# Kernel tuning notes

Measured on AMD Instinct MI355X. Metric: run time of the kernel, lower is better.

## Reference

```python
import jax, jax.numpy as jnp
import numpy as np

H, DH, HID = 8, 16, 128
N_USER, N_ITEM, N_TASTE, N_IMAGE = 20000, 50000, 50000, 50000


def setup_inputs() -> dict:
    key = jax.random.key(0)
    ks = jax.random.split(key, 24)
    f = jax.random.normal
    s = 1.0 / np.sqrt(HID).astype(np.float32)
    inp = {
        "x_user": f(ks[0], (N_USER, HID), jnp.float32),
        "x_item": f(ks[1], (N_ITEM, HID), jnp.float32),
        "x_taste": f(ks[2], (N_TASTE, HID), jnp.float32),
        "x_image": f(ks[3], (N_IMAGE, HID), jnp.float32),
        "Wk": f(ks[4], (4, HID, HID), jnp.float32) * s,
        "bk": jnp.zeros((4, HID), jnp.float32),
        "Wq": f(ks[5], (4, HID, HID), jnp.float32) * s,
        "bq": jnp.zeros((4, HID), jnp.float32),
        "Wv": f(ks[6], (4, HID, HID), jnp.float32) * s,
        "bv": jnp.zeros((4, HID), jnp.float32),
        "a_rel": f(ks[7], (4, H, DH, DH), jnp.float32) * (1.0 / np.sqrt(DH).astype(np.float32)),
        "m_rel": f(ks[8], (4, H, DH, DH), jnp.float32) * (1.0 / np.sqrt(DH).astype(np.float32)),
        "p_rel": jnp.ones((4, H), jnp.float32),
        "Wo": f(ks[9], (2, HID, HID), jnp.float32) * s,
        "bo": jnp.zeros((2, HID), jnp.float32),
        "skip": jnp.ones((2,), jnp.float32),
        "ti_src": jax.random.randint(ks[10], (50000,), 0, N_TASTE, jnp.int32),
        "ti_dst": jax.random.randint(ks[11], (50000,), 0, N_ITEM, jnp.int32),
        "im_src": jax.random.randint(ks[12], (50000,), 0, N_IMAGE, jnp.int32),
        "im_dst": jax.random.randint(ks[13], (50000,), 0, N_ITEM, jnp.int32),
        "ub_src": jax.random.randint(ks[14], (500000,), 0, N_USER, jnp.int32),
        "ub_dst": jax.random.randint(ks[15], (500000,), 0, N_ITEM, jnp.int32),
        "bu_src": jax.random.randint(ks[16], (500000,), 0, N_ITEM, jnp.int32),
        "bu_dst": jax.random.randint(ks[17], (500000,), 0, N_USER, jnp.int32),
    }
    return inp


def _kqv(x, i, Wk, bk, Wq, bq, Wv, bv):
    k = (x @ Wk[i] + bk[i]).reshape(-1, H, DH)
    q = (x @ Wq[i] + bq[i]).reshape(-1, H, DH)
    v = (x @ Wv[i] + bv[i]).reshape(-1, H, DH)
    return k, q, v


def _edge_alpha_msg(k_src, v_src, q_dst, src, dst, a, m, p):
    # per-edge-type relation transform at node level, then gather per edge
    kr = jnp.einsum('nhd,hde->nhe', k_src, a)  # [Nsrc,H,DH]
    vr = jnp.einsum('nhd,hde->nhe', v_src, m)
    alpha = (q_dst[dst] * kr[src]).sum(-1) * p * (1.0 / np.sqrt(DH).astype(np.float32))  # [E,H]
    return alpha, vr[src]


def _seg_softmax_agg(alpha, msg, dst, n):
    amax = jax.ops.segment_max(alpha, dst, num_segments=n)
    amax = jnp.where(jnp.isfinite(amax), amax, 0.0)
    ex = jnp.exp(alpha - amax[dst])
    den = jax.ops.segment_sum(ex, dst, num_segments=n)
    w = ex / (den[dst] + 1e-16)
    return jax.ops.segment_sum(msg * w[..., None], dst, num_segments=n)  # [n,H,DH]


def reference(x_user, x_item, x_taste, x_image, Wk, bk, Wq, bq, Wv, bv,
              a_rel, m_rel, p_rel, Wo, bo, skip,
              ti_src, ti_dst, im_src, im_dst, ub_src, ub_dst, bu_src, bu_dst):
    k_u, q_u, v_u = _kqv(x_user, 0, Wk, bk, Wq, bq, Wv, bv)
    k_i, q_i, v_i = _kqv(x_item, 1, Wk, bk, Wq, bq, Wv, bv)
    k_t, _, v_t = _kqv(x_taste, 2, Wk, bk, Wq, bq, Wv, bv)
    k_g, _, v_g = _kqv(x_image, 3, Wk, bk, Wq, bq, Wv, bv)

    # edges into 'item': taste(0), image(1), user-buys(2); softmax over all combined per item
    a0, m0 = _edge_alpha_msg(k_t, v_t, q_i, ti_src, ti_dst, a_rel[0], m_rel[0], p_rel[0])
    a1, m1 = _edge_alpha_msg(k_g, v_g, q_i, im_src, im_dst, a_rel[1], m_rel[1], p_rel[1])
    a2, m2 = _edge_alpha_msg(k_u, v_u, q_i, ub_src, ub_dst, a_rel[2], m_rel[2], p_rel[2])
    alpha_i = jnp.concatenate([a0, a1, a2], 0)
    msg_i = jnp.concatenate([m0, m1, m2], 0)
    dst_i = jnp.concatenate([ti_dst, im_dst, ub_dst], 0)
    agg_i = _seg_softmax_agg(alpha_i, msg_i, dst_i, N_ITEM)

    # edges into 'user': item-bought_by(3)
    a3, m3 = _edge_alpha_msg(k_i, v_i, q_u, bu_src, bu_dst, a_rel[3], m_rel[3], p_rel[3])
    agg_u = _seg_softmax_agg(a3, m3, bu_dst, N_USER)

    out_i = jax.nn.gelu(agg_i.reshape(-1, HID), approximate=False) @ Wo[0] + bo[0]
    g_i = jax.nn.sigmoid(skip[0])
    out_i = g_i * out_i + (1.0 - g_i) * x_item

    out_u = jax.nn.gelu(agg_u.reshape(-1, HID), approximate=False) @ Wo[1] + bo[1]
    g_u = jax.nn.sigmoid(skip[1])
    out_u = g_u * out_u + (1.0 - g_u) * x_user
    return (out_i, out_u)
```

## Files before the change

kernel.cpp:

```cpp
#include <hip/hip_runtime.h>
#include <math.h>


namespace {
constexpr int HIDN  = 128;
constexpr int NHEAD = 8;

constexpr int NU = 20000, NI = 50000, NT = 50000, NG = 50000;
constexpr int E_TI = 50000, E_IM = 50000, E_UB = 500000, E_BU = 500000;
constexpr int ETOT = E_TI + E_IM + E_UB + E_BU;
constexpr int ND   = NI + NU;

constexpr int BASE_U = 0;
constexpr int BASE_I = NU;
constexpr int BASE_T = NU + NI;
constexpr int BASE_G = NU + NI + NT;

constexpr int NMAT = 12;
constexpr int MATSZ = 128 * 128;
constexpr int SU = 136;

constexpr int NBU = (NU + 63) / 64;
constexpr int NBI = (NI + 63) / 64;
constexpr int NBT = (NT + 63) / 64;
constexpr int NBG = (NG + 63) / 64;
}

typedef __attribute__((ext_vector_type(8))) short short8v;
typedef __attribute__((ext_vector_type(4))) float f32x4;
typedef __attribute__((ext_vector_type(4))) unsigned short ushort4v;

__device__ __forceinline__ unsigned short bf16rne(float f) {
    unsigned u = __float_as_uint(f);
    unsigned r = (u + 0x7fffu + ((u >> 16) & 1u)) >> 16;
    return (unsigned short)r;
}
__device__ __forceinline__ float bf16f(unsigned short h) {
    return __uint_as_float(((unsigned)h) << 16);
}
__device__ __forceinline__ float bflo(unsigned int u) { return __uint_as_float(u << 16); }
__device__ __forceinline__ float bfhi(unsigned int u) { return __uint_as_float(u & 0xffff0000u); }

__global__ void build_cw_kernel(const float* __restrict__ Wk, const float* __restrict__ bk,
                                const float* __restrict__ Wv, const float* __restrict__ bv,
                                const float* __restrict__ a_rel, const float* __restrict__ m_rel,
                                const float* __restrict__ p_rel,
                                float* __restrict__ cw)
{
    const int total = 2 * 4 * 129 * 128;
    int idx = blockIdx.x * blockDim.x + threadIdx.x;
    if (idx >= total) return;
    int c     = idx & 127;
    int r     = (idx >> 7) % 129;
    int t     = ((idx >> 7) / 129) & 3;
    int which = idx / (4 * 129 * 128);
    const int et_map[4] = {2, 3, 0, 1};
    int et = et_map[t];
    const float* W = (which == 0 ? Wk : Wv) + (size_t)t * HIDN * HIDN;
    const float* b = (which == 0 ? bk : bv) + (size_t)t * HIDN;
    const float* A = (which == 0 ? a_rel : m_rel) + (size_t)et * NHEAD * 16 * 16;
    int h = c >> 4, e2 = c & 15;
    float s = 0.f;
#pragma unroll
    for (int d = 0; d < 16; ++d) {
        float w = (r == 128) ? b[h * 16 + d] : W[(size_t)r * HIDN + h * 16 + d];
        s = fmaf(w, A[h * 256 + d * 16 + e2], s);
    }
    if (which == 0) s *= p_rel[et * NHEAD + h] * 0.25f;
    cw[idx] = s;
}

__global__ void pack_kernel(const float* __restrict__ cw,
                            const float* __restrict__ Wq, const float* __restrict__ bq,
                            const float* __restrict__ Wo, const float* __restrict__ bo,
                            short* __restrict__ pkh, short* __restrict__ pkl,
                            float* __restrict__ bias)
{
    const int total = NMAT * MATSZ + NMAT * HIDN;
    int idx = blockIdx.x * blockDim.x + threadIdx.x;
    if (idx >= total) return;
    if (idx < NMAT * MATSZ) {
        int mat = idx >> 14;
        int rem = idx & (MATSZ - 1);
        int i    = rem & 7;
        int lane = (rem >> 3) & 63;
        int ct   = (rem >> 9) & 7;
        int ks   = rem >> 12;
        int k   = ks * 32 + ((lane >> 4) & 3) * 8 + i;
        int col = ct * 16 + (lane & 15);
        float v;
        if (mat < 8)       v = cw[(size_t)mat * 129 * 128 + (size_t)k * 128 + col];
        else if (mat < 10) v = Wq[(size_t)(mat - 8) * MATSZ + (size_t)k * 128 + col];
        else               v = Wo[(size_t)(mat - 10) * MATSZ + (size_t)k * 128 + col];
        unsigned short hb = bf16rne(v);
        float rest = v - bf16f(hb);
        pkh[idx] = (short)hb;
        pkl[idx] = (short)bf16rne(rest);
    } else {
        int b = idx - NMAT * MATSZ;
        int mat = b >> 7, col = b & 127;
        float v;
        if (mat < 8)       v = cw[(size_t)mat * 129 * 128 + (size_t)128 * 128 + col];
        else if (mat < 10) v = bq[(mat - 8) * HIDN + col];
        else               v = bo[(mat - 10) * HIDN + col];
        bias[b] = v;
    }
}

__global__ __launch_bounds__(256) void mfma_proj_all(
    const float* __restrict__ xu, const float* __restrict__ xi,
    const float* __restrict__ xt, const float* __restrict__ xg,
    const short* __restrict__ pkh, const short* __restrict__ pkl,
    const float* __restrict__ bias,
    unsigned short* __restrict__ krb, unsigned short* __restrict__ vrb,
    unsigned short* __restrict__ qb_u, unsigned short* __restrict__ qb_i)
{
    int b = blockIdx.x;
    int seg, bloc;
    if (b < NBU)                  { seg = 0; bloc = b; }
    else if (b < NBU + NBI)       { seg = 1; bloc = b - NBU; }
    else if (b < NBU + NBI + NBT) { seg = 2; bloc = b - NBU - NBI; }
    else                          { seg = 3; bloc = b - NBU - NBI - NBT; }
    const float* x = (seg == 0) ? xu : (seg == 1) ? xi : (seg == 2) ? xt : xg;
    const int M     = (seg == 0) ? NU : (seg == 1) ? NI : (seg == 2) ? NT : NG;
    const int rbase = (seg == 0) ? BASE_U : (seg == 1) ? BASE_I : (seg == 2) ? BASE_T : BASE_G;
    unsigned short* qp = (seg == 0) ? qb_u : (seg == 1) ? qb_i : nullptr;

    __shared__ unsigned short hs[64 * SU];
    __shared__ unsigned short ls[64 * SU];
    const int t  = threadIdx.x;
    const int r0 = bloc * 64;
    const int rows = min(64, M - r0);

#pragma unroll
    for (int p = 0; p < 8; ++p) {
        int f = p * 256 + t;
        int row = f >> 5, c4 = f & 31;
        float4 v = make_float4(0.f, 0.f, 0.f, 0.f);
        if (row < rows) v = *(const float4*)(x + (size_t)(r0 + row) * HIDN + c4 * 4);
        float vv[4] = {v.x, v.y, v.z, v.w};
        ushort4v hq, lq;
#pragma unroll
        for (int i = 0; i < 4; ++i) {
            unsigned short hb = bf16rne(vv[i]);
            hq[i] = hb;
            lq[i] = bf16rne(vv[i] - bf16f(hb));
        }
        *(ushort4v*)&hs[row * SU + c4 * 4] = hq;
        *(ushort4v*)&ls[row * SU + c4 * 4] = lq;
    }
    __syncthreads();

    const int l = t & 63, w = t >> 6;
    const int kgrp = l >> 4;
    const int ct0  = 2 * w;
    const int ccol = l & 15;

    for (int mi = 0; mi < 3; ++mi) {
        if (mi == 2 && qp == nullptr) break;
        const int mat = (mi == 0) ? seg : (mi == 1) ? (4 + seg) : (8 + seg);
        const short8v* bh = (const short8v*)(pkh + (size_t)mat * MATSZ);
        const short8v* bl = (const short8v*)(pkl + (size_t)mat * MATSZ);
        const float*   bs = bias + mat * HIDN;

        short8v B1[4][2], B2[4][2];
#pragma unroll
        for (int ks = 0; ks < 4; ++ks) {
#pragma unroll
            for (int c = 0; c < 2; ++c) {
                B1[ks][c] = bh[(ks * 8 + ct0 + c) * 64 + l];
                if (mi == 2) B2[ks][c] = bl[(ks * 8 + ct0 + c) * 64 + l];
            }
        }

        const float bv0 = bs[(ct0 + 0) * 16 + ccol];
        const float bv1 = bs[(ct0 + 1) * 16 + ccol];

        for (int rt = 0; rt < 4; ++rt) {
            f32x4 a0, a1;
            a0[0]=0.f;a0[1]=0.f;a0[2]=0.f;a0[3]=0.f;
            a1[0]=0.f;a1[1]=0.f;a1[2]=0.f;a1[3]=0.f;
            const int arow = rt * 16 + ccol;
#pragma unroll
            for (int ks = 0; ks < 4; ++ks) {
                short8v ah = *(const short8v*)&hs[arow * SU + ks * 32 + kgrp * 8];
                short8v al = *(const short8v*)&ls[arow * SU + ks * 32 + kgrp * 8];
                a0 = __builtin_amdgcn_mfma_f32_16x16x32_bf16(ah, B1[ks][0], a0, 0, 0, 0);
                a1 = __builtin_amdgcn_mfma_f32_16x16x32_bf16(ah, B1[ks][1], a1, 0, 0, 0);
                a0 = __builtin_amdgcn_mfma_f32_16x16x32_bf16(al, B1[ks][0], a0, 0, 0, 0);
                a1 = __builtin_amdgcn_mfma_f32_16x16x32_bf16(al, B1[ks][1], a1, 0, 0, 0);
                if (mi == 2) {
                    a0 = __builtin_amdgcn_mfma_f32_16x16x32_bf16(ah, B2[ks][0], a0, 0, 0, 0);
                    a1 = __builtin_amdgcn_mfma_f32_16x16x32_bf16(ah, B2[ks][1], a1, 0, 0, 0);
                }
            }
            const int crow = r0 + rt * 16 + kgrp * 4;
            unsigned short* dst = (mi == 0) ? krb + (size_t)rbase * HIDN
                                : (mi == 1) ? vrb + (size_t)rbase * HIDN
                                            : qp;
#pragma unroll
            for (int j = 0; j < 4; ++j) {
                int grow = crow + j;
                if (grow < M) {
                    size_t o = (size_t)grow * HIDN;
                    dst[o + (ct0 + 0) * 16 + ccol] = bf16rne(a0[j] + bv0);
                    dst[o + (ct0 + 1) * 16 + ccol] = bf16rne(a1[j] + bv1);
                }
            }
        }
    }
}

__global__ __launch_bounds__(256) void mfma_out_all(
    const float* __restrict__ agg_i, const float* __restrict__ agg_u,
    const short* __restrict__ pkh, const short* __restrict__ pkl,
    const float* __restrict__ bias,
    const float* __restrict__ x_item, const float* __restrict__ x_user,
    const float* __restrict__ skip_ptr,
    float* __restrict__ outp)
{
    int b = blockIdx.x;
    int seg = (b < NBI) ? 0 : 1;
    int bloc = (seg == 0) ? b : b - NBI;
    const float* agg = (seg == 0) ? agg_i : agg_u;
    const float* xin = (seg == 0) ? x_item : x_user;
    const int M = (seg == 0) ? NI : NU;
    const int mat = 10 + seg;
    float* out = (seg == 0) ? outp : outp + (size_t)NI * HIDN;

    __shared__ unsigned short hs[64 * SU];
    __shared__ unsigned short ls[64 * SU];
    const int t  = threadIdx.x;
    const int r0 = bloc * 64;
    const int rows = min(64, M - r0);

#pragma unroll
    for (int p = 0; p < 8; ++p) {
        int f = p * 256 + t;
        int row = f >> 5, c4 = f & 31;
        float4 v = make_float4(0.f, 0.f, 0.f, 0.f);
        if (row < rows) v = *(const float4*)(agg + (size_t)(r0 + row) * HIDN + c4 * 4);
        float vv[4] = {v.x, v.y, v.z, v.w};
        ushort4v hq, lq;
#pragma unroll
        for (int i = 0; i < 4; ++i) {
            float g = 0.5f * vv[i] * (1.0f + erff(vv[i] * 0.70710678118654752440f));
            unsigned short hb = bf16rne(g);
            hq[i] = hb;
            lq[i] = bf16rne(g - bf16f(hb));
        }
        *(ushort4v*)&hs[row * SU + c4 * 4] = hq;
        *(ushort4v*)&ls[row * SU + c4 * 4] = lq;
    }
    __syncthreads();

    const int l = t & 63, w = t >> 6;
    const int kgrp = l >> 4;
    const int ct0  = 2 * w;
    const int ccol = l & 15;

    const short8v* bh = (const short8v*)(pkh + (size_t)mat * MATSZ);
    const short8v* bl = (const short8v*)(pkl + (size_t)mat * MATSZ);
    const float*   bs = bias + mat * HIDN;

    short8v B1[4][2], B2[4][2];
#pragma unroll
    for (int ks = 0; ks < 4; ++ks) {
#pragma unroll
        for (int c = 0; c < 2; ++c) {
            B1[ks][c] = bh[(ks * 8 + ct0 + c) * 64 + l];
            B2[ks][c] = bl[(ks * 8 + ct0 + c) * 64 + l];
        }
    }

    const float gate = 1.f / (1.f + expf(-skip_ptr[seg]));
    const float og = 1.f - gate;
    const float bv0 = bs[(ct0 + 0) * 16 + ccol];
    const float bv1 = bs[(ct0 + 1) * 16 + ccol];

    for (int rt = 0; rt < 4; ++rt) {
        f32x4 a0, a1;
        a0[0]=0.f;a0[1]=0.f;a0[2]=0.f;a0[3]=0.f;
        a1[0]=0.f;a1[1]=0.f;a1[2]=0.f;a1[3]=0.f;
        const int arow = rt * 16 + ccol;
#pragma unroll
        for (int ks = 0; ks < 4; ++ks) {
            short8v ah = *(const short8v*)&hs[arow * SU + ks * 32 + kgrp * 8];
            short8v al = *(const short8v*)&ls[arow * SU + ks * 32 + kgrp * 8];
            a0 = __builtin_amdgcn_mfma_f32_16x16x32_bf16(ah, B1[ks][0], a0, 0, 0, 0);
            a1 = __builtin_amdgcn_mfma_f32_16x16x32_bf16(ah, B1[ks][1], a1, 0, 0, 0);
            a0 = __builtin_amdgcn_mfma_f32_16x16x32_bf16(al, B1[ks][0], a0, 0, 0, 0);
            a1 = __builtin_amdgcn_mfma_f32_16x16x32_bf16(al, B1[ks][1], a1, 0, 0, 0);
            a0 = __builtin_amdgcn_mfma_f32_16x16x32_bf16(ah, B2[ks][0], a0, 0, 0, 0);
            a1 = __builtin_amdgcn_mfma_f32_16x16x32_bf16(ah, B2[ks][1], a1, 0, 0, 0);
        }
        const int crow = r0 + rt * 16 + kgrp * 4;
#pragma unroll
        for (int j = 0; j < 4; ++j) {
            int grow = crow + j;
            if (grow < M) {
                size_t o = (size_t)grow * HIDN;
                size_t o0 = o + (ct0 + 0) * 16 + ccol;
                size_t o1 = o + (ct0 + 1) * 16 + ccol;
                out[o0] = gate * (a0[j] + bv0) + og * xin[o0];
                out[o1] = gate * (a1[j] + bv1) + og * xin[o1];
            }
        }
    }
}


__global__ void hist_kernel(const int* __restrict__ ti_dst, const int* __restrict__ im_dst,
                            const int* __restrict__ ub_dst, const int* __restrict__ bu_dst,
                            int* __restrict__ deg)
{
    int i = blockIdx.x * blockDim.x + threadIdx.x;
    if (i >= ETOT) return;
    int d;
    if (i < E_TI)                     d = ti_dst[i];
    else if (i < E_TI + E_IM)         d = im_dst[i - E_TI];
    else if (i < E_TI + E_IM + E_UB)  d = ub_dst[i - E_TI - E_IM];
    else                              d = NI + bu_dst[i - E_TI - E_IM - E_UB];
    atomicAdd(&deg[d], 1);
}

__global__ void scan1_kernel(int* __restrict__ deg, int* __restrict__ tops, int n)
{
    __shared__ int sh[256];
    int i = blockIdx.x * 256 + threadIdx.x;
    int v = (i < n) ? deg[i] : 0;
    sh[threadIdx.x] = v;
    __syncthreads();
    for (int o = 1; o < 256; o <<= 1) {
        int t = (threadIdx.x >= o) ? sh[threadIdx.x - o] : 0;
        __syncthreads();
        sh[threadIdx.x] += t;
        __syncthreads();
    }
    if (i < n) deg[i] = sh[threadIdx.x];
    if (threadIdx.x == 255) tops[blockIdx.x] = sh[255];
}

__global__ void scan2_kernel(int* __restrict__ tops, int nb)
{
    __shared__ int sh[1024];
    int v = (threadIdx.x < nb) ? tops[threadIdx.x] : 0;
    sh[threadIdx.x] = v;
    __syncthreads();
    for (int o = 1; o < 1024; o <<= 1) {
        int t = (threadIdx.x >= o) ? sh[threadIdx.x - o] : 0;
        __syncthreads();
        sh[threadIdx.x] += t;
        __syncthreads();
    }
    if (threadIdx.x < nb) tops[threadIdx.x] = sh[threadIdx.x];
}

__global__ void scan3_kernel(const int* __restrict__ part, const int* __restrict__ tops,
                             int* __restrict__ rowptr, int* __restrict__ cursor, int n)
{
    int i = blockIdx.x * 256 + threadIdx.x;
    if (i >= n) return;
    int add = (blockIdx.x > 0) ? tops[blockIdx.x - 1] : 0;
    int prev = (i > 0) ? ((threadIdx.x > 0) ? part[i - 1] + add
                                            : ((blockIdx.x > 0) ? tops[blockIdx.x - 1] : 0))
                       : 0;
    rowptr[i + 1] = part[i] + add;
    cursor[i] = prev;
    if (i == 0) rowptr[0] = 0;
}

__global__ void scatter_kernel(const int* __restrict__ ti_src, const int* __restrict__ ti_dst,
                               const int* __restrict__ im_src, const int* __restrict__ im_dst,
                               const int* __restrict__ ub_src, const int* __restrict__ ub_dst,
                               const int* __restrict__ bu_src, const int* __restrict__ bu_dst,
                               int* __restrict__ cursor, int* __restrict__ col)
{
    int i = blockIdx.x * blockDim.x + threadIdx.x;
    if (i >= ETOT) return;
    int d, row;
    if (i < E_TI)                    { d = ti_dst[i];                  row = BASE_T + ti_src[i]; }
    else if (i < E_TI + E_IM)        { int e = i - E_TI;               row = BASE_G + im_src[e]; d = im_dst[e]; }
    else if (i < E_TI + E_IM + E_UB) { int e = i - E_TI - E_IM;        row = BASE_U + ub_src[e]; d = ub_dst[e]; }
    else                             { int e = i - E_TI - E_IM - E_UB; row = BASE_I + bu_src[e]; d = NI + bu_dst[e]; }
    int p = atomicAdd(&cursor[d], 1);
    col[p] = row;
}

__global__ __launch_bounds__(256) void f12_kernel(
    const int* __restrict__ rowptr, const int* __restrict__ rowend,
    const int* __restrict__ col,
    const unsigned int* __restrict__ krw,
    const unsigned int* __restrict__ qb_i, const unsigned int* __restrict__ qb_u,
    const unsigned int* __restrict__ vrw,
    float* __restrict__ agg_i, float* __restrict__ agg_u)
{
    int wid = (blockIdx.x << 2) + (threadIdx.x >> 6);
    if (wid >= ND) return;
    const int l = threadIdx.x & 63;

    unsigned int qu = (wid < NI) ? qb_i[(size_t)wid * 64 + l]
                                 : qb_u[(size_t)(wid - NI) * 64 + l];
    const float qx = bflo(qu), qy = bfhi(qu);

    const int start = rowptr[wid], end = rowend[wid];
    float m = -3.0e38f, ax = 0.f, ay = 0.f, den = 0.f;

    int p = start;
    for (; p + 3 < end; p += 4) {
        int r0_ = col[p], r1_ = col[p + 1], r2_ = col[p + 2], r3_ = col[p + 3];
        unsigned int u0 = krw[(size_t)r0_ * 64 + l];
        unsigned int u1 = krw[(size_t)r1_ * 64 + l];
        unsigned int u2 = krw[(size_t)r2_ * 64 + l];
        unsigned int u3 = krw[(size_t)r3_ * 64 + l];
        unsigned int v0 = vrw[(size_t)r0_ * 64 + l];
        unsigned int v1 = vrw[(size_t)r1_ * 64 + l];
        unsigned int v2 = vrw[(size_t)r2_ * 64 + l];
        unsigned int v3 = vrw[(size_t)r3_ * 64 + l];
        float d0 = qx * bflo(u0) + qy * bfhi(u0);
        float d1 = qx * bflo(u1) + qy * bfhi(u1);
        float d2 = qx * bflo(u2) + qy * bfhi(u2);
        float d3 = qx * bflo(u3) + qy * bfhi(u3);
        d0 += __shfl_xor(d0, 1); d1 += __shfl_xor(d1, 1);
        d2 += __shfl_xor(d2, 1); d3 += __shfl_xor(d3, 1);
        d0 += __shfl_xor(d0, 2); d1 += __shfl_xor(d1, 2);
        d2 += __shfl_xor(d2, 2); d3 += __shfl_xor(d3, 2);
        d0 += __shfl_xor(d0, 4); d1 += __shfl_xor(d1, 4);
        d2 += __shfl_xor(d2, 4); d3 += __shfl_xor(d3, 4);
        float mn = fmaxf(m, fmaxf(fmaxf(d0, d1), fmaxf(d2, d3)));
        float s  = __expf(m - mn);
        float e0 = __expf(d0 - mn);
        float e1 = __expf(d1 - mn);
        float e2 = __expf(d2 - mn);
        float e3 = __expf(d3 - mn);
        ax = ax * s + e0 * bflo(v0) + e1 * bflo(v1) + e2 * bflo(v2) + e3 * bflo(v3);
        ay = ay * s + e0 * bfhi(v0) + e1 * bfhi(v1) + e2 * bfhi(v2) + e3 * bfhi(v3);
        den = den * s + (e0 + e1) + (e2 + e3);
        m = mn;
    }
    for (; p < end; ++p) {
        int r0_ = col[p];
        unsigned int u0 = krw[(size_t)r0_ * 64 + l];
        unsigned int v0 = vrw[(size_t)r0_ * 64 + l];
        float d0 = qx * bflo(u0) + qy * bfhi(u0);
        d0 += __shfl_xor(d0, 1);
        d0 += __shfl_xor(d0, 2);
        d0 += __shfl_xor(d0, 4);
        float mn = fmaxf(m, d0);
        float s  = __expf(m - mn);
        float e0 = __expf(d0 - mn);
        ax = ax * s + e0 * bflo(v0);
        ay = ay * s + e0 * bfhi(v0);
        den = den * s + e0;
        m = mn;
    }

    float inv = 1.f / (den + 1e-16f);
    float* dst = (wid < NI) ? agg_i + (size_t)wid * HIDN
                            : agg_u + (size_t)(wid - NI) * HIDN;
    *(float2*)(dst + 2 * l) = make_float2(ax * inv, ay * inv);
}

extern "C" void kernel_launch(void* const* d_in, const int* in_sizes, int n_in,
                              void* d_out, int out_size, void* d_ws, size_t ws_size,
                              hipStream_t stream)
{
    const float* x_user = (const float*)d_in[0];
    const float* x_item = (const float*)d_in[1];
    const float* x_taste= (const float*)d_in[2];
    const float* x_image= (const float*)d_in[3];
    const float* Wk     = (const float*)d_in[4];
    const float* bk     = (const float*)d_in[5];
    const float* Wq     = (const float*)d_in[6];
    const float* bq     = (const float*)d_in[7];
    const float* Wv     = (const float*)d_in[8];
    const float* bv     = (const float*)d_in[9];
    const float* a_rel  = (const float*)d_in[10];
    const float* m_rel  = (const float*)d_in[11];
    const float* p_rel  = (const float*)d_in[12];
    const float* Wo     = (const float*)d_in[13];
    const float* bo     = (const float*)d_in[14];
    const float* skip   = (const float*)d_in[15];
    const int* ti_src = (const int*)d_in[16];
    const int* ti_dst = (const int*)d_in[17];
    const int* im_src = (const int*)d_in[18];
    const int* im_dst = (const int*)d_in[19];
    const int* ub_src = (const int*)d_in[20];
    const int* ub_dst = (const int*)d_in[21];
    const int* bu_src = (const int*)d_in[22];
    const int* bu_dst = (const int*)d_in[23];

    float* ws = (float*)d_ws;
    float* outp = (float*)d_out;
    (void)in_sizes; (void)n_in; (void)out_size;

    size_t off = 0;
    auto alloc = [&](size_t n) { size_t o = off; off += n; return o; };
    const size_t o_cw   = alloc((size_t)2 * 4 * 129 * 128);
    const size_t o_pkh  = alloc((size_t)NMAT * MATSZ / 2);
    const size_t o_pkl  = alloc((size_t)NMAT * MATSZ / 2);
    const size_t o_bias = alloc((size_t)NMAT * HIDN);
    const size_t o_krb  = alloc((size_t)(NU + NI + NT + NG) * HIDN / 2);
    const size_t o_vrb  = alloc((size_t)(NU + NI + NT + NG) * HIDN / 2);
    const size_t o_q_i  = alloc((size_t)NI * HIDN / 2);
    const size_t o_q_u  = alloc((size_t)NU * HIDN / 2);
    const size_t o_agg  = alloc((size_t)(NI + NU) * HIDN);
    const size_t o_int  = alloc((size_t)(ND + 1) + ND + 1024 + ETOT);

    if (ws_size < off * sizeof(float)) return;

    unsigned short* krb  = (unsigned short*)(ws + o_krb);
    unsigned short* vrb  = (unsigned short*)(ws + o_vrb);
    unsigned short* qb_i = (unsigned short*)(ws + o_q_i);
    unsigned short* qb_u = (unsigned short*)(ws + o_q_u);

    short* pkh  = (short*)(ws + o_pkh);
    short* pkl  = (short*)(ws + o_pkl);
    float* bias = ws + o_bias;

    int* deg    = (int*)(ws + o_cw);
    int* rowptr = (int*)(ws + o_int);
    int* cursor = rowptr + (ND + 1);
    int* tops   = cursor + ND;
    int* col    = tops + 1024;

    float* agg_i = ws + o_agg;
    float* agg_u = ws + o_agg + (size_t)NI * HIDN;

    {
        int total = 2 * 4 * 129 * 128;
        build_cw_kernel<<<(total + 255) / 256, 256, 0, stream>>>(
            Wk, bk, Wv, bv, a_rel, m_rel, p_rel, ws + o_cw);
        int ptotal = NMAT * MATSZ + NMAT * HIDN;
        pack_kernel<<<(ptotal + 255) / 256, 256, 0, stream>>>(
            ws + o_cw, Wq, bq, Wo, bo, pkh, pkl, bias);
    }

    mfma_proj_all<<<NBU + NBI + NBT + NBG, 256, 0, stream>>>(
        x_user, x_item, x_taste, x_image, pkh, pkl, bias,
        krb, vrb, qb_u, qb_i);

    hipMemsetAsync(deg, 0, ND * sizeof(int), stream);
    hist_kernel<<<(ETOT + 255) / 256, 256, 0, stream>>>(ti_dst, im_dst, ub_dst, bu_dst, deg);
    const int NB1 = (ND + 255) / 256;
    scan1_kernel<<<NB1, 256, 0, stream>>>(deg, tops, ND);
    scan2_kernel<<<1, 1024, 0, stream>>>(tops, NB1);
    scan3_kernel<<<NB1, 256, 0, stream>>>(deg, tops, rowptr, cursor, ND);
    scatter_kernel<<<(ETOT + 255) / 256, 256, 0, stream>>>(
        ti_src, ti_dst, im_src, im_dst, ub_src, ub_dst, bu_src, bu_dst, cursor, col);

    const int NBW = (ND + 3) / 4;
    f12_kernel<<<NBW, 256, 0, stream>>>(
        rowptr, cursor, col,
        (const unsigned int*)krb, (const unsigned int*)qb_i, (const unsigned int*)qb_u,
        (const unsigned int*)vrb,
        agg_i, agg_u);

    mfma_out_all<<<NBI + NBU, 256, 0, stream>>>(
        agg_i, agg_u, pkh, pkl, bias, x_item, x_user, skip, outp);
}
```

Measured before the change: 328.4 us.

## Fuse weight-build, memset and histogram into other kernels; store aggregates as bf16

The relation-weight composition now happens inside the pack kernel, and the degree memset is folded into that same kernel, which drops a launch and a memset. The edge-degree histogram runs as extra blocks appended to the projection kernel, so it overlaps with the GEMM work. The aggregation output is stored in bf16 instead of fp32, halving its write and read traffic. The bf16 rounding of the aggregates adds precision loss before the output projection.

```diff
diff --git a/kernel.cpp b/kernel.cpp
--- a/kernel.cpp
+++ b/kernel.cpp
@@ -24,6 +24,8 @@
 constexpr int NBI = (NI + 63) / 64;
 constexpr int NBT = (NT + 63) / 64;
 constexpr int NBG = (NG + 63) / 64;
+constexpr int NPROJ = NBU + NBI + NBT + NBG;
+constexpr int NBH   = (ETOT + 255) / 256;
 }
 
 typedef __attribute__((ext_vector_type(8))) short short8v;
@@ -41,45 +43,19 @@
 __device__ __forceinline__ float bflo(unsigned int u) { return __uint_as_float(u << 16); }
 __device__ __forceinline__ float bfhi(unsigned int u) { return __uint_as_float(u & 0xffff0000u); }
 
-__global__ void build_cw_kernel(const float* __restrict__ Wk, const float* __restrict__ bk,
-                                const float* __restrict__ Wv, const float* __restrict__ bv,
-                                const float* __restrict__ a_rel, const float* __restrict__ m_rel,
-                                const float* __restrict__ p_rel,
-                                float* __restrict__ cw)
-{
-    const int total = 2 * 4 * 129 * 128;
-    int idx = blockIdx.x * blockDim.x + threadIdx.x;
-    if (idx >= total) return;
-    int c     = idx & 127;
-    int r     = (idx >> 7) % 129;
-    int t     = ((idx >> 7) / 129) & 3;
-    int which = idx / (4 * 129 * 128);
-    const int et_map[4] = {2, 3, 0, 1};
-    int et = et_map[t];
-    const float* W = (which == 0 ? Wk : Wv) + (size_t)t * HIDN * HIDN;
-    const float* b = (which == 0 ? bk : bv) + (size_t)t * HIDN;
-    const float* A = (which == 0 ? a_rel : m_rel) + (size_t)et * NHEAD * 16 * 16;
-    int h = c >> 4, e2 = c & 15;
-    float s = 0.f;
-#pragma unroll
-    for (int d = 0; d < 16; ++d) {
-        float w = (r == 128) ? b[h * 16 + d] : W[(size_t)r * HIDN + h * 16 + d];
-        s = fmaf(w, A[h * 256 + d * 16 + e2], s);
-    }
-    if (which == 0) s *= p_rel[et * NHEAD + h] * 0.25f;
-    cw[idx] = s;
-}
-
-__global__ void pack_kernel(const float* __restrict__ cw,
+__global__ void pack_kernel(const float* __restrict__ Wk, const float* __restrict__ bk,
+                            const float* __restrict__ Wv, const float* __restrict__ bv,
+                            const float* __restrict__ a_rel, const float* __restrict__ m_rel,
+                            const float* __restrict__ p_rel,
                             const float* __restrict__ Wq, const float* __restrict__ bq,
                             const float* __restrict__ Wo, const float* __restrict__ bo,
                             short* __restrict__ pkh, short* __restrict__ pkl,
-                            float* __restrict__ bias)
-{
-    const int total = NMAT * MATSZ + NMAT * HIDN;
+                            float* __restrict__ bias, int* __restrict__ deg)
+{
+    const int NW = NMAT * MATSZ;
+    const int NB = NMAT * HIDN;
     int idx = blockIdx.x * blockDim.x + threadIdx.x;
-    if (idx >= total) return;
-    if (idx < NMAT * MATSZ) {
+    if (idx < NW) {
         int mat = idx >> 14;
         int rem = idx & (MATSZ - 1);
         int i    = rem & 7;
@@ -89,21 +65,51 @@
         int k   = ks * 32 + ((lane >> 4) & 3) * 8 + i;
         int col = ct * 16 + (lane & 15);
         float v;
-        if (mat < 8)       v = cw[(size_t)mat * 129 * 128 + (size_t)k * 128 + col];
-        else if (mat < 10) v = Wq[(size_t)(mat - 8) * MATSZ + (size_t)k * 128 + col];
-        else               v = Wo[(size_t)(mat - 10) * MATSZ + (size_t)k * 128 + col];
+        if (mat < 8) {
+            int which = mat >> 2;
+            int tt = mat & 3;
+            const int et_map[4] = {2, 3, 0, 1};
+            int et = et_map[tt];
+            const float* W = (which == 0 ? Wk : Wv) + (size_t)tt * MATSZ;
+            const float* A = (which == 0 ? a_rel : m_rel) + (size_t)et * NHEAD * 256;
+            int h = ct, e2 = col & 15;
+            float s = 0.f;
+#pragma unroll
+            for (int d = 0; d < 16; ++d)
+                s = fmaf(W[(size_t)k * HIDN + h * 16 + d], A[h * 256 + d * 16 + e2], s);
+            if (which == 0) s *= p_rel[et * NHEAD + h] * 0.25f;
+            v = s;
+        } else if (mat < 10) {
+            v = Wq[(size_t)(mat - 8) * MATSZ + (size_t)k * HIDN + col];
+        } else {
+            v = Wo[(size_t)(mat - 10) * MATSZ + (size_t)k * HIDN + col];
+        }
         unsigned short hb = bf16rne(v);
-        float rest = v - bf16f(hb);
         pkh[idx] = (short)hb;
-        pkl[idx] = (short)bf16rne(rest);
-    } else {
-        int b = idx - NMAT * MATSZ;
+        pkl[idx] = (short)bf16rne(v - bf16f(hb));
+    } else if (idx < NW + NB) {
+        int b = idx - NW;
         int mat = b >> 7, col = b & 127;
         float v;
-        if (mat < 8)       v = cw[(size_t)mat * 129 * 128 + (size_t)128 * 128 + col];
-        else if (mat < 10) v = bq[(mat - 8) * HIDN + col];
-        else               v = bo[(mat - 10) * HIDN + col];
+        if (mat < 8) {
+            int which = mat >> 2;
+            int tt = mat & 3;
+            const int et_map[4] = {2, 3, 0, 1};
+            int et = et_map[tt];
+            const float* bb = (which == 0 ? bk : bv) + tt * HIDN;
+            const float* A  = (which == 0 ? a_rel : m_rel) + (size_t)et * NHEAD * 256;
+            int h = col >> 4, e2 = col & 15;
+            float s = 0.f;
+#pragma unroll
+            for (int d = 0; d < 16; ++d)
+                s = fmaf(bb[h * 16 + d], A[h * 256 + d * 16 + e2], s);
+            if (which == 0) s *= p_rel[et * NHEAD + h] * 0.25f;
+            v = s;
+        } else if (mat < 10) v = bq[(mat - 8) * HIDN + col];
+        else                 v = bo[(mat - 10) * HIDN + col];
         bias[b] = v;
+    } else if (idx < NW + NB + ND) {
+        deg[idx - NW - NB] = 0;
     }
 }
 
@@ -113,9 +119,25 @@
     const short* __restrict__ pkh, const short* __restrict__ pkl,
     const float* __restrict__ bias,
     unsigned short* __restrict__ krb, unsigned short* __restrict__ vrb,
-    unsigned short* __restrict__ qb_u, unsigned short* __restrict__ qb_i)
+    unsigned short* __restrict__ qb_u, unsigned short* __restrict__ qb_i,
+    const int* __restrict__ ti_dst, const int* __restrict__ im_dst,
+    const int* __restrict__ ub_dst, const int* __restrict__ bu_dst,
+    int* __restrict__ deg)
 {
     int b = blockIdx.x;
+    if (b >= NPROJ) {
+        int i = (b - NPROJ) * 256 + threadIdx.x;
+        if (i < ETOT) {
+            int d;
+            if (i < E_TI)                     d = ti_dst[i];
+            else if (i < E_TI + E_IM)         d = im_dst[i - E_TI];
+            else if (i < E_TI + E_IM + E_UB)  d = ub_dst[i - E_TI - E_IM];
+            else                              d = NI + bu_dst[i - E_TI - E_IM - E_UB];
+            atomicAdd(&deg[d], 1);
+        }
+        return;
+    }
+
     int seg, bloc;
     if (b < NBU)                  { seg = 0; bloc = b; }
     else if (b < NBU + NBI)       { seg = 1; bloc = b - NBU; }
@@ -212,7 +234,7 @@
 }
 
 __global__ __launch_bounds__(256) void mfma_out_all(
-    const float* __restrict__ agg_i, const float* __restrict__ agg_u,
+    const unsigned short* __restrict__ agg_i, const unsigned short* __restrict__ agg_u,
     const short* __restrict__ pkh, const short* __restrict__ pkl,
     const float* __restrict__ bias,
     const float* __restrict__ x_item, const float* __restrict__ x_user,
@@ -222,7 +244,7 @@
     int b = blockIdx.x;
     int seg = (b < NBI) ? 0 : 1;
     int bloc = (seg == 0) ? b : b - NBI;
-    const float* agg = (seg == 0) ? agg_i : agg_u;
+    const unsigned short* agg = (seg == 0) ? agg_i : agg_u;
     const float* xin = (seg == 0) ? x_item : x_user;
     const int M = (seg == 0) ? NI : NU;
     const int mat = 10 + seg;
@@ -238,9 +260,12 @@
     for (int p = 0; p < 8; ++p) {
         int f = p * 256 + t;
         int row = f >> 5, c4 = f & 31;
-        float4 v = make_float4(0.f, 0.f, 0.f, 0.f);
-        if (row < rows) v = *(const float4*)(agg + (size_t)(r0 + row) * HIDN + c4 * 4);
-        float vv[4] = {v.x, v.y, v.z, v.w};
+        float vv[4] = {0.f, 0.f, 0.f, 0.f};
+        if (row < rows) {
+            uint2 u = *(const uint2*)(agg + (size_t)(r0 + row) * HIDN + c4 * 4);
+            vv[0] = bflo(u.x); vv[1] = bfhi(u.x);
+            vv[2] = bflo(u.y); vv[3] = bfhi(u.y);
+        }
         ushort4v hq, lq;
 #pragma unroll
         for (int i = 0; i < 4; ++i) {
@@ -309,20 +334,6 @@
     }
 }
 
-
-__global__ void hist_kernel(const int* __restrict__ ti_dst, const int* __restrict__ im_dst,
-                            const int* __restrict__ ub_dst, const int* __restrict__ bu_dst,
-                            int* __restrict__ deg)
-{
-    int i = blockIdx.x * blockDim.x + threadIdx.x;
-    if (i >= ETOT) return;
-    int d;
-    if (i < E_TI)                     d = ti_dst[i];
-    else if (i < E_TI + E_IM)         d = im_dst[i - E_TI];
-    else if (i < E_TI + E_IM + E_UB)  d = ub_dst[i - E_TI - E_IM];
-    else                              d = NI + bu_dst[i - E_TI - E_IM - E_UB];
-    atomicAdd(&deg[d], 1);
-}
 
 __global__ void scan1_kernel(int* __restrict__ deg, int* __restrict__ tops, int n)
 {
@@ -393,7 +404,7 @@
     const unsigned int* __restrict__ krw,
     const unsigned int* __restrict__ qb_i, const unsigned int* __restrict__ qb_u,
     const unsigned int* __restrict__ vrw,
-    float* __restrict__ agg_i, float* __restrict__ agg_u)
+    unsigned short* __restrict__ agg_i, unsigned short* __restrict__ agg_u)
 {
     int wid = (blockIdx.x << 2) + (threadIdx.x >> 6);
     if (wid >= ND) return;
@@ -456,9 +467,10 @@
     }
 
     float inv = 1.f / (den + 1e-16f);
-    float* dst = (wid < NI) ? agg_i + (size_t)wid * HIDN
-                            : agg_u + (size_t)(wid - NI) * HIDN;
-    *(float2*)(dst + 2 * l) = make_float2(ax * inv, ay * inv);
+    unsigned short* dst = (wid < NI) ? agg_i + (size_t)wid * HIDN
+                                     : agg_u + (size_t)(wid - NI) * HIDN;
+    unsigned int packed = (unsigned)bf16rne(ax * inv) | ((unsigned)bf16rne(ay * inv) << 16);
+    *(unsigned int*)(dst + 2 * l) = packed;
 }
 
 extern "C" void kernel_launch(void* const* d_in, const int* in_sizes, int n_in,
@@ -496,7 +508,6 @@
 
     size_t off = 0;
     auto alloc = [&](size_t n) { size_t o = off; off += n; return o; };
-    const size_t o_cw   = alloc((size_t)2 * 4 * 129 * 128);
     const size_t o_pkh  = alloc((size_t)NMAT * MATSZ / 2);
     const size_t o_pkl  = alloc((size_t)NMAT * MATSZ / 2);
     const size_t o_bias = alloc((size_t)NMAT * HIDN);
@@ -504,8 +515,8 @@
     const size_t o_vrb  = alloc((size_t)(NU + NI + NT + NG) * HIDN / 2);
     const size_t o_q_i  = alloc((size_t)NI * HIDN / 2);
     const size_t o_q_u  = alloc((size_t)NU * HIDN / 2);
-    const size_t o_agg  = alloc((size_t)(NI + NU) * HIDN);
-    const size_t o_int  = alloc((size_t)(ND + 1) + ND + 1024 + ETOT);
+    const size_t o_agg  = alloc((size_t)(NI + NU) * HIDN / 2);
+    const size_t o_int  = alloc((size_t)(ND + 1) + ND + 1024 + ETOT + ND);
 
     if (ws_size < off * sizeof(float)) return;
 
@@ -518,30 +529,27 @@
     short* pkl  = (short*)(ws + o_pkl);
     float* bias = ws + o_bias;
 
-    int* deg    = (int*)(ws + o_cw);
     int* rowptr = (int*)(ws + o_int);
     int* cursor = rowptr + (ND + 1);
     int* tops   = cursor + ND;
     int* col    = tops + 1024;
-
-    float* agg_i = ws + o_agg;
-    float* agg_u = ws + o_agg + (size_t)NI * HIDN;
+    int* deg    = col + ETOT;
+
+    unsigned short* agg_i = (unsigned short*)(ws + o_agg);
+    unsigned short* agg_u = agg_i + (size_t)NI * HIDN;
 
     {
-        int total = 2 * 4 * 129 * 128;
-        build_cw_kernel<<<(total + 255) / 256, 256, 0, stream>>>(
-            Wk, bk, Wv, bv, a_rel, m_rel, p_rel, ws + o_cw);
-        int ptotal = NMAT * MATSZ + NMAT * HIDN;
+        int ptotal = NMAT * MATSZ + NMAT * HIDN + ND;
         pack_kernel<<<(ptotal + 255) / 256, 256, 0, stream>>>(
-            ws + o_cw, Wq, bq, Wo, bo, pkh, pkl, bias);
-    }
-
-    mfma_proj_all<<<NBU + NBI + NBT + NBG, 256, 0, stream>>>(
+            Wk, bk, Wv, bv, a_rel, m_rel, p_rel, Wq, bq, Wo, bo,
+            pkh, pkl, bias, deg);
+    }
+
+    mfma_proj_all<<<NPROJ + NBH, 256, 0, stream>>>(
         x_user, x_item, x_taste, x_image, pkh, pkl, bias,
-        krb, vrb, qb_u, qb_i);
-
-    hipMemsetAsync(deg, 0, ND * sizeof(int), stream);
-    hist_kernel<<<(ETOT + 255) / 256, 256, 0, stream>>>(ti_dst, im_dst, ub_dst, bu_dst, deg);
+        krb, vrb, qb_u, qb_i,
+        ti_dst, im_dst, ub_dst, bu_dst, deg);
+
     const int NB1 = (ND + 255) / 256;
     scan1_kernel<<<NB1, 256, 0, stream>>>(deg, tops, ND);
     scan2_kernel<<<1, 1024, 0, stream>>>(tops, NB1);
```

Result: faster. 299.0 us (median of 2 runs) (-8.9%).
